# Kernel optimization log

Hardware: AMD Instinct MI355X
Metric: run time of the kernel (lower is better)

## Reference

```python
import jax, jax.numpy as jnp
import numpy as np

GCN_DIM = 512
POS_EMB_DIM = 64
K = 8
L = 128  # uttr_len
B = 16
PAIR_FEAT = 2 * GCN_DIM + POS_EMB_DIM


def _pair_indices(L, K):
    # Static (trace-time) construction of the windowed pair list, matching the
    # torch masked_select over the full L*L pair grid: row p = i*L + j keeps
    # pairs with |j - i| <= K, in the same row-major order.
    i = np.repeat(np.arange(L), L)
    j = np.tile(np.arange(L), L)
    rel = j - i
    mask = np.abs(rel) <= K
    return i[mask], j[mask], rel[mask]


def setup_inputs() -> dict:
    key = jax.random.key(0)
    k1, k2, k3, k4, k5, k6, k7 = jax.random.split(key, 7)
    h_emo = jax.random.normal(k1, (B, L, GCN_DIM), dtype=jnp.float32)
    h_cause = jax.random.normal(k2, (B, L, GCN_DIM), dtype=jnp.float32)
    # xavier_uniform for embedding table
    lim_e = np.sqrt(6.0 / (2 * K + 1 + POS_EMB_DIM))
    pos_emb = jax.random.uniform(k3, (2 * K + 1, POS_EMB_DIM), minval=-lim_e, maxval=lim_e, dtype=jnp.float32)
    lim1 = np.sqrt(1.0 / PAIR_FEAT)
    W1 = jax.random.uniform(k4, (PAIR_FEAT, PAIR_FEAT), minval=-lim1, maxval=lim1, dtype=jnp.float32)
    b1 = jax.random.uniform(k5, (PAIR_FEAT,), minval=-lim1, maxval=lim1, dtype=jnp.float32)
    W2 = jax.random.uniform(k6, (1, PAIR_FEAT), minval=-lim1, maxval=lim1, dtype=jnp.float32)
    b2 = jax.random.uniform(k7, (1,), minval=-lim1, maxval=lim1, dtype=jnp.float32)
    return {
        "uttr_output_h_emotion": h_emo,
        "uttr_output_h_cause": h_cause,
        "pos_emb": pos_emb,
        "W1": W1,
        "b1": b1,
        "W2": W2,
        "b2": b2,
    }


def reference(uttr_output_h_emotion, uttr_output_h_cause, pos_emb, W1, b1, W2, b2):
    emo_idx, cau_idx, rel_np = _pair_indices(L, K)  # static numpy, length n
    emo_idx_j = jnp.asarray(emo_idx)
    cau_idx_j = jnp.asarray(cau_idx)
    rel = jnp.asarray(rel_np)  # [n], values in [-K, K]

    # windowed pair gather: couples_h = [H_emo[i] ; H_cause[j]]  -> [B, n, 2*g]
    P = jnp.concatenate(
        [uttr_output_h_emotion[:, emo_idx_j, :], uttr_output_h_cause[:, cau_idx_j, :]],
        axis=2,
    )

    # relative-position embedding + Gaussian kernel smoothing (batch-invariant)
    rel_emb = pos_emb[rel + K]  # [n, pos_emb_dim]
    rel_f = rel.astype(jnp.float32)
    kernel = jnp.exp(-jnp.square(rel_f[:, None] - rel_f[None, :]))  # [n, n]
    smoothed = kernel @ rel_emb  # [n, pos_emb_dim]

    couples = jnp.concatenate(
        [P, jnp.broadcast_to(smoothed[None], (P.shape[0],) + smoothed.shape)], axis=2
    )  # [B, n, PAIR_FEAT]

    h = jax.nn.relu(jnp.einsum("bnf,gf->bng", couples, W1) + b1)
    pred = (jnp.einsum("bnf,of->bno", h, W2) + b2).squeeze(-1)  # [B, n]

    emo_cau_pos = jnp.stack([emo_idx_j + 1, cau_idx_j + 1], axis=1)  # [n, 2], int
    return pred, emo_cau_pos
```

## Files before the change

kernel.cpp:

```cpp
#include <hip/hip_runtime.h>

typedef unsigned short u16;
typedef unsigned int u32;
typedef __attribute__((ext_vector_type(4))) float f32x4;
typedef __attribute__((ext_vector_type(8))) __bf16 bf16x8;
typedef __attribute__((ext_vector_type(4))) u16 u16x4;
typedef __attribute__((ext_vector_type(4))) float f32x4v;

#define LSEQ 128
#define KW 8
#define NP 2104
#define BATCH 16
#define MTOT 33664
#define FDIM 1088
#define GPAD 1152

#define WS_W1P  0ul
#define WS_EMOB 2506752ul
#define WS_CAUB 4603904ul
#define WS_SB   6701056ul
#define WS_TABI 6775040ul
#define WS_TABJ 6783456ul
#define WS_TABR 6791872ul
#define WS_EC   6800288ul

__device__ __forceinline__ u16 f2bf(float x) {
  union { float f; u32 u; } v; v.f = x;
  u32 r = v.u + 0x7fffu + ((v.u >> 16) & 1u);
  return (u16)(r >> 16);
}

__device__ __forceinline__ void load_lds16(const void* g, void* l) {
  __builtin_amdgcn_global_load_lds(
      (const __attribute__((address_space(1))) void*)g,
      (__attribute__((address_space(3))) void*)l, 16, 0, 0);
}

__global__ __launch_bounds__(256)
void setup_all(const float* __restrict__ emo, const float* __restrict__ cau,
               const float* __restrict__ pos_emb, const float* __restrict__ W1,
               const float* __restrict__ b1,
               u16* __restrict__ W1p, u16* __restrict__ emoB,
               u16* __restrict__ cauB, float* __restrict__ Sb,
               int* __restrict__ tab_i, int* __restrict__ tab_j,
               int* __restrict__ tab_r, float* __restrict__ out_pos) {
  __shared__ float smL[17 * 64];
  const int bx = blockIdx.x;
  const int t = threadIdx.x;
  if (bx < 1224) {
    int idx = bx * 256 + t;
    if (idx >= 313344) return;
    int g = idx / 272;
    int f = (idx - g * 272) * 4;
    u16x4 o;
    if (g < 1088) {
      f32x4v v = *(const f32x4v*)&W1[g * 1088 + f];
      o.x = f2bf(v.x); o.y = f2bf(v.y); o.z = f2bf(v.z); o.w = f2bf(v.w);
    } else {
      o.x = 0; o.y = 0; o.z = 0; o.w = 0;
    }
    *(u16x4*)&W1p[(size_t)g * 1088 + f] = o;
  } else if (bx < 3272) {
    int idx = (bx - 1224) * 256 + t;
    if (idx < 262144) {
      f32x4v v = *(const f32x4v*)&emo[idx * 4];
      u16x4 o; o.x = f2bf(v.x); o.y = f2bf(v.y); o.z = f2bf(v.z); o.w = f2bf(v.w);
      *(u16x4*)&emoB[idx * 4] = o;
    } else {
      int k = idx - 262144;
      f32x4v v = *(const f32x4v*)&cau[k * 4];
      u16x4 o; o.x = f2bf(v.x); o.y = f2bf(v.y); o.z = f2bf(v.z); o.w = f2bf(v.w);
      *(u16x4*)&cauB[k * 4] = o;
    }
  } else if (bx == 3272) {
    if (t < LSEQ) {
      int i = t;
      int off = 0;
      for (int tt = 0; tt < i; ++tt) {
        int lo = tt - KW; if (lo < 0) lo = 0;
        int hi = tt + KW; if (hi > LSEQ - 1) hi = LSEQ - 1;
        off += hi - lo + 1;
      }
      int jlo = i - KW; if (jlo < 0) jlo = 0;
      int jhi = i + KW; if (jhi > LSEQ - 1) jhi = LSEQ - 1;
      for (int j = jlo; j <= jhi; ++j) {
        int p = off + (j - jlo);
        tab_i[p] = i; tab_j[p] = j; tab_r[p] = j - i;
        out_pos[2 * p]     = (float)(i + 1);
        out_pos[2 * p + 1] = (float)(j + 1);
      }
    }
  } else {
    for (int idx = t; idx < 17 * 64; idx += 256) {
      int r = idx >> 6, d = idx & 63;
      float acc = 0.f;
      for (int s = 0; s < 17; ++s) {
        float diff = (float)(r - s);
        int a = s - 8; if (a < 0) a = -a;
        float cnt = (float)(128 - a);
        acc += cnt * expf(-diff * diff) * pos_emb[s * 64 + d];
      }
      smL[idx] = acc;
    }
    __syncthreads();
    int idx2 = (bx - 3273) * 256 + t;
    if (idx2 < 17 * 1088) {
      int r = idx2 / 1088;
      int g = idx2 - r * 1088;
      float a = b1[g];
      const float* wr = &W1[(size_t)g * 1088 + 1024];
      const float* sr = &smL[r * 64];
#pragma unroll 8
      for (int d = 0; d < 64; ++d) a = fmaf(sr[d], wr[d], a);
      Sb[r * 1088 + g] = a;
    }
  }
}

__global__ __launch_bounds__(256, 2)
void feat_gemm(const u16* __restrict__ emoB, const u16* __restrict__ cauB,
               const u16* __restrict__ W1p, float* __restrict__ EC) {
  __shared__ __align__(16) u16 As[128 * 32];
  __shared__ __align__(16) u16 Bs[128 * 32];

  const int tid = threadIdx.x;
  const int mblk = blockIdx.x;
  const int gbase = blockIdx.y * 128;

  const int lane = tid & 63;
  const int w = tid >> 6;
  const int lrow = lane & 15;
  const int lk = (lane >> 4) * 8;
  const int wm = (w >> 1) * 64;
  const int wn = (w & 1) * 64;

  const int row0 = tid >> 2;
  const int sub = (tid & 3) * 8;

  const u16* Asrc = (mblk < 16) ? emoB : cauB;
  const int arow = (mblk & 15) * 128;
  const int fsel = (mblk < 16) ? 0 : 512;

  const u32 a0 = (u32)(arow + row0) * 512 + sub;
  const u32 a1 = a0 + 64 * 512;
  const u32 b0 = (u32)(gbase + row0) * 1088 + fsel + sub;
  const u32 b1o = b0 + 64 * 1088;

  char* AsB = (char*)&As[0] + w * 1024;
  char* BsB = (char*)&Bs[0] + w * 1024;

  f32x4 acc[4][4];
#pragma unroll
  for (int mi = 0; mi < 4; ++mi)
#pragma unroll
    for (int ni = 0; ni < 4; ++ni) acc[mi][ni] = (f32x4){0.f, 0.f, 0.f, 0.f};

  for (int ks = 0; ks < 16; ++ks) {
    const int f0 = ks * 32;
    load_lds16(Asrc + a0 + f0, AsB);
    load_lds16(Asrc + a1 + f0, AsB + 4096);
    load_lds16(W1p + b0 + f0, BsB);
    load_lds16(W1p + b1o + f0, BsB + 4096);
    __syncthreads();

    bf16x8 av[4], bv[4];
#pragma unroll
    for (int mi = 0; mi < 4; ++mi)
      av[mi] = *(const bf16x8*)&As[(wm + mi * 16 + lrow) * 32 + lk];
#pragma unroll
    for (int ni = 0; ni < 4; ++ni)
      bv[ni] = *(const bf16x8*)&Bs[(wn + ni * 16 + lrow) * 32 + lk];
#pragma unroll
    for (int mi = 0; mi < 4; ++mi)
#pragma unroll
      for (int ni = 0; ni < 4; ++ni)
        acc[mi][ni] = __builtin_amdgcn_mfma_f32_16x16x32_bf16(av[mi], bv[ni], acc[mi][ni], 0, 0, 0);
    __syncthreads();
  }

  const int rbase = mblk * 128 + wm + ((lane >> 4) << 2);
#pragma unroll
  for (int mi = 0; mi < 4; ++mi) {
#pragma unroll
    for (int ni = 0; ni < 4; ++ni) {
      const int ocol = gbase + wn + ni * 16 + lrow;
      float* dst = EC + (size_t)(rbase + mi * 16) * GPAD + ocol;
#pragma unroll
      for (int r2 = 0; r2 < 4; ++r2) dst[(size_t)r2 * GPAD] = acc[mi][ni][r2];
    }
  }
}

__global__ __launch_bounds__(256)
void combine(const float* __restrict__ EC, const float* __restrict__ Sb,
             const float* __restrict__ W2, const float* __restrict__ b2,
             const int* __restrict__ tab_i, const int* __restrict__ tab_j,
             const int* __restrict__ tab_r, float* __restrict__ pred) {
  const int bid = blockIdx.x;
  const int sb = (bid & 7) * 1052 + (bid >> 3);
  const int w = threadIdx.x >> 6;
  const int lane = threadIdx.x & 63;
  const int q = sb * 4 + w;
  const int b = q / NP;
  const int p = q - b * NP;
  const int i = tab_i[p];
  const int j = tab_j[p];
  const int r = tab_r[p];

  const float* e = EC + (size_t)(b * LSEQ + i) * GPAD;
  const float* c = EC + (size_t)(2048 + b * LSEQ + j) * GPAD;
  const float* s = Sb + (r + KW) * FDIM;

  f32x4v acc = {0.f, 0.f, 0.f, 0.f};
#pragma unroll
  for (int it = 0; it < 4; ++it) {
    const int g = it * 256 + (lane << 2);
    f32x4v ev = *(const f32x4v*)(e + g);
    f32x4v cv = *(const f32x4v*)(c + g);
    f32x4v sv = *(const f32x4v*)(s + g);
    f32x4v wv = *(const f32x4v*)(W2 + g);
    float v0 = fmaxf(ev.x + cv.x + sv.x, 0.f);
    float v1 = fmaxf(ev.y + cv.y + sv.y, 0.f);
    float v2 = fmaxf(ev.z + cv.z + sv.z, 0.f);
    float v3 = fmaxf(ev.w + cv.w + sv.w, 0.f);
    acc.x = fmaf(v0, wv.x, acc.x);
    acc.y = fmaf(v1, wv.y, acc.y);
    acc.z = fmaf(v2, wv.z, acc.z);
    acc.w = fmaf(v3, wv.w, acc.w);
  }
  float a = acc.x + acc.y + acc.z + acc.w;
  {
    const int g = 1024 + lane;
    float v = fmaxf(e[g] + c[g] + s[g], 0.f);
    a = fmaf(v, W2[g], a);
  }
  a += __shfl_xor(a, 1);
  a += __shfl_xor(a, 2);
  a += __shfl_xor(a, 4);
  a += __shfl_xor(a, 8);
  a += __shfl_xor(a, 16);
  a += __shfl_xor(a, 32);
  if (lane == 0) pred[q] = a + b2[0];
}

extern "C" void kernel_launch(void* const* d_in, const int* in_sizes, int n_in,
                              void* d_out, int out_size, void* d_ws, size_t ws_size,
                              hipStream_t stream) {
  const float* h_emo = (const float*)d_in[0];
  const float* h_cau = (const float*)d_in[1];
  const float* pos_emb = (const float*)d_in[2];
  const float* W1 = (const float*)d_in[3];
  const float* b1 = (const float*)d_in[4];
  const float* W2 = (const float*)d_in[5];
  const float* b2 = (const float*)d_in[6];

  char* ws = (char*)d_ws;
  u16* W1p = (u16*)(ws + WS_W1P);
  u16* emoB = (u16*)(ws + WS_EMOB);
  u16* cauB = (u16*)(ws + WS_CAUB);
  float* Sb = (float*)(ws + WS_SB);
  int* tab_i = (int*)(ws + WS_TABI);
  int* tab_j = (int*)(ws + WS_TABJ);
  int* tab_r = (int*)(ws + WS_TABR);
  float* EC = (float*)(ws + WS_EC);

  float* pred = (float*)d_out;
  float* out_pos = (float*)d_out + MTOT;

  setup_all<<<3346, 256, 0, stream>>>(h_emo, h_cau, pos_emb, W1, b1,
                                      W1p, emoB, cauB, Sb,
                                      tab_i, tab_j, tab_r, out_pos);
  feat_gemm<<<dim3(32, 9), 256, 0, stream>>>(emoB, cauB, W1p, EC);
  combine<<<8416, 256, 0, stream>>>(EC, Sb, W2, b2, tab_i, tab_j, tab_r, pred);
}
```

Baseline: 120.3 us.

## Restructure combine per query row with LDS-staged bf16 bias table and smaller GEMM tiles

The combine kernel now assigns one emotion row i per pair of waves. Each wave keeps its E row and W2 slice in registers and iterates over the window of cause rows j with a software-prefetched next row. The 17x1088 smoothed-bias table is stored as bf16 and staged into LDS per block, replacing per-pair index tables with a single row-offset table. The feature GEMM M tile is halved to 64 rows to double the block count and raise occupancy. This cuts redundant E and W2 global reads and raises GEMM parallelism, at the cost of bf16 rounding on the bias term, a large LDS allocation per combine block, and serial loops inside each block.

```diff
diff --git a/kernel.cpp b/kernel.cpp
--- a/kernel.cpp
+++ b/kernel.cpp
@@ -19,15 +19,17 @@
 #define WS_EMOB 2506752ul
 #define WS_CAUB 4603904ul
 #define WS_SB   6701056ul
-#define WS_TABI 6775040ul
-#define WS_TABJ 6783456ul
-#define WS_TABR 6791872ul
-#define WS_EC   6800288ul
+#define WS_TOFF 6738048ul
+#define WS_EC   6738560ul
 
 __device__ __forceinline__ u16 f2bf(float x) {
   union { float f; u32 u; } v; v.f = x;
   u32 r = v.u + 0x7fffu + ((v.u >> 16) & 1u);
   return (u16)(r >> 16);
+}
+
+__device__ __forceinline__ float bf2f(u16 x) {
+  union { u32 u; float f; } v; v.u = ((u32)x) << 16; return v.f;
 }
 
 __device__ __forceinline__ void load_lds16(const void* g, void* l) {
@@ -41,9 +43,8 @@
                const float* __restrict__ pos_emb, const float* __restrict__ W1,
                const float* __restrict__ b1,
                u16* __restrict__ W1p, u16* __restrict__ emoB,
-               u16* __restrict__ cauB, float* __restrict__ Sb,
-               int* __restrict__ tab_i, int* __restrict__ tab_j,
-               int* __restrict__ tab_r, float* __restrict__ out_pos) {
+               u16* __restrict__ cauB, u16* __restrict__ Sb,
+               int* __restrict__ tab_off, float* __restrict__ out_pos) {
   __shared__ float smL[17 * 64];
   const int bx = blockIdx.x;
   const int t = threadIdx.x;
@@ -81,11 +82,11 @@
         int hi = tt + KW; if (hi > LSEQ - 1) hi = LSEQ - 1;
         off += hi - lo + 1;
       }
+      tab_off[i] = off;
       int jlo = i - KW; if (jlo < 0) jlo = 0;
       int jhi = i + KW; if (jhi > LSEQ - 1) jhi = LSEQ - 1;
       for (int j = jlo; j <= jhi; ++j) {
         int p = off + (j - jlo);
-        tab_i[p] = i; tab_j[p] = j; tab_r[p] = j - i;
         out_pos[2 * p]     = (float)(i + 1);
         out_pos[2 * p + 1] = (float)(j + 1);
       }
@@ -112,15 +113,15 @@
       const float* sr = &smL[r * 64];
 #pragma unroll 8
       for (int d = 0; d < 64; ++d) a = fmaf(sr[d], wr[d], a);
-      Sb[r * 1088 + g] = a;
-    }
-  }
-}
-
-__global__ __launch_bounds__(256, 2)
+      Sb[r * 1088 + g] = f2bf(a);
+    }
+  }
+}
+
+__global__ __launch_bounds__(256, 4)
 void feat_gemm(const u16* __restrict__ emoB, const u16* __restrict__ cauB,
                const u16* __restrict__ W1p, float* __restrict__ EC) {
-  __shared__ __align__(16) u16 As[128 * 32];
+  __shared__ __align__(16) u16 As[64 * 32];
   __shared__ __align__(16) u16 Bs[128 * 32];
 
   const int tid = threadIdx.x;
@@ -131,56 +132,54 @@
   const int w = tid >> 6;
   const int lrow = lane & 15;
   const int lk = (lane >> 4) * 8;
-  const int wm = (w >> 1) * 64;
+  const int wm = (w >> 1) * 32;
   const int wn = (w & 1) * 64;
 
   const int row0 = tid >> 2;
   const int sub = (tid & 3) * 8;
 
-  const u16* Asrc = (mblk < 16) ? emoB : cauB;
-  const int arow = (mblk & 15) * 128;
-  const int fsel = (mblk < 16) ? 0 : 512;
+  const u16* Asrc = (mblk < 32) ? emoB : cauB;
+  const int arow = (mblk & 31) * 64;
+  const int fsel = (mblk < 32) ? 0 : 512;
 
   const u32 a0 = (u32)(arow + row0) * 512 + sub;
-  const u32 a1 = a0 + 64 * 512;
   const u32 b0 = (u32)(gbase + row0) * 1088 + fsel + sub;
-  const u32 b1o = b0 + 64 * 1088;
-
-  char* AsB = (char*)&As[0] + w * 1024;
-  char* BsB = (char*)&Bs[0] + w * 1024;
-
-  f32x4 acc[4][4];
-#pragma unroll
-  for (int mi = 0; mi < 4; ++mi)
+  const u32 b1o = b0 + 64u * 1088;
+
+  char* AsD = (char*)&As[0] + tid * 16;
+  char* BsD = (char*)&Bs[0] + tid * 16;
+
+  f32x4 acc[2][4];
+#pragma unroll
+  for (int mi = 0; mi < 2; ++mi)
 #pragma unroll
     for (int ni = 0; ni < 4; ++ni) acc[mi][ni] = (f32x4){0.f, 0.f, 0.f, 0.f};
 
   for (int ks = 0; ks < 16; ++ks) {
     const int f0 = ks * 32;
-    load_lds16(Asrc + a0 + f0, AsB);
-    load_lds16(Asrc + a1 + f0, AsB + 4096);
-    load_lds16(W1p + b0 + f0, BsB);
-    load_lds16(W1p + b1o + f0, BsB + 4096);
+    load_lds16(Asrc + a0 + f0, AsD);
+    load_lds16(W1p + b0 + f0, BsD);
+    load_lds16(W1p + b1o + f0, BsD + 4096);
     __syncthreads();
 
-    bf16x8 av[4], bv[4];
-#pragma unroll
-    for (int mi = 0; mi < 4; ++mi)
+    bf16x8 av[2], bv[4];
+#pragma unroll
+    for (int mi = 0; mi < 2; ++mi)
       av[mi] = *(const bf16x8*)&As[(wm + mi * 16 + lrow) * 32 + lk];
 #pragma unroll
     for (int ni = 0; ni < 4; ++ni)
       bv[ni] = *(const bf16x8*)&Bs[(wn + ni * 16 + lrow) * 32 + lk];
 #pragma unroll
-    for (int mi = 0; mi < 4; ++mi)
+    for (int mi = 0; mi < 2; ++mi)
 #pragma unroll
       for (int ni = 0; ni < 4; ++ni)
         acc[mi][ni] = __builtin_amdgcn_mfma_f32_16x16x32_bf16(av[mi], bv[ni], acc[mi][ni], 0, 0, 0);
     __syncthreads();
   }
 
-  const int rbase = mblk * 128 + wm + ((lane >> 4) << 2);
-#pragma unroll
-  for (int mi = 0; mi < 4; ++mi) {
+  const int rbase = mblk * 64 + wm + ((lane >> 4) << 2);
+#pragma unroll
+  for (int mi = 0; mi < 2; ++mi) {
 #pragma unroll
     for (int ni = 0; ni < 4; ++ni) {
       const int ocol = gbase + wn + ni * 16 + lrow;
@@ -191,56 +190,110 @@
   }
 }
 
-__global__ __launch_bounds__(256)
-void combine(const float* __restrict__ EC, const float* __restrict__ Sb,
+__global__ __launch_bounds__(256, 4)
+void combine(const float* __restrict__ EC, const u16* __restrict__ Sb,
              const float* __restrict__ W2, const float* __restrict__ b2,
-             const int* __restrict__ tab_i, const int* __restrict__ tab_j,
-             const int* __restrict__ tab_r, float* __restrict__ pred) {
+             const int* __restrict__ tab_off, float* __restrict__ pred) {
+  __shared__ __align__(16) u16 Sl[17 * 1088];
+  __shared__ float partA[2][17], partB[2][17];
+
+  const int tid = threadIdx.x;
   const int bid = blockIdx.x;
-  const int sb = (bid & 7) * 1052 + (bid >> 3);
-  const int w = threadIdx.x >> 6;
-  const int lane = threadIdx.x & 63;
-  const int q = sb * 4 + w;
-  const int b = q / NP;
-  const int p = q - b * NP;
-  const int i = tab_i[p];
-  const int j = tab_j[p];
-  const int r = tab_r[p];
-
-  const float* e = EC + (size_t)(b * LSEQ + i) * GPAD;
-  const float* c = EC + (size_t)(2048 + b * LSEQ + j) * GPAD;
-  const float* s = Sb + (r + KW) * FDIM;
-
-  f32x4v acc = {0.f, 0.f, 0.f, 0.f};
-#pragma unroll
-  for (int it = 0; it < 4; ++it) {
-    const int g = it * 256 + (lane << 2);
-    f32x4v ev = *(const f32x4v*)(e + g);
-    f32x4v cv = *(const f32x4v*)(c + g);
-    f32x4v sv = *(const f32x4v*)(s + g);
-    f32x4v wv = *(const f32x4v*)(W2 + g);
-    float v0 = fmaxf(ev.x + cv.x + sv.x, 0.f);
-    float v1 = fmaxf(ev.y + cv.y + sv.y, 0.f);
-    float v2 = fmaxf(ev.z + cv.z + sv.z, 0.f);
-    float v3 = fmaxf(ev.w + cv.w + sv.w, 0.f);
-    acc.x = fmaf(v0, wv.x, acc.x);
-    acc.y = fmaf(v1, wv.y, acc.y);
-    acc.z = fmaf(v2, wv.z, acc.z);
-    acc.w = fmaf(v3, wv.w, acc.w);
-  }
-  float a = acc.x + acc.y + acc.z + acc.w;
+  const int sb = (bid & 7) * 128 + (bid >> 3);
+
   {
-    const int g = 1024 + lane;
-    float v = fmaxf(e[g] + c[g] + s[g], 0.f);
-    a = fmaf(v, W2[g], a);
-  }
-  a += __shfl_xor(a, 1);
-  a += __shfl_xor(a, 2);
-  a += __shfl_xor(a, 4);
-  a += __shfl_xor(a, 8);
-  a += __shfl_xor(a, 16);
-  a += __shfl_xor(a, 32);
-  if (lane == 0) pred[q] = a + b2[0];
+    char* dst = (char*)&Sl[0];
+    const char* src = (const char*)Sb;
+#pragma unroll
+    for (int it = 0; it < 9; ++it)
+      load_lds16(src + it * 4096 + tid * 16, dst + it * 4096 + tid * 16);
+    if (tid < 8)
+      load_lds16(src + 36864 + tid * 16, dst + 36864 + tid * 16);
+  }
+
+  const int w = tid >> 6;
+  const int lane = tid & 63;
+  const int h = w >> 1;
+  const int gh = w & 1;
+  const int u = sb * 2 + h;
+  const int b = u >> 7;
+  const int i = u & 127;
+  int jlo = i - KW; if (jlo < 0) jlo = 0;
+  int jhi = i + KW; if (jhi > 127) jhi = 127;
+
+  const float bias2 = b2[0];
+  const float* Erow = EC + (size_t)(b * 128 + i) * GPAD;
+  const float* Cbase = EC + (size_t)(2048 + b * 128) * GPAD;
+
+  const int g0 = gh * 512 + lane * 4;
+  const int g1 = g0 + 256;
+  const f32x4v e0 = *(const f32x4v*)(Erow + g0);
+  const f32x4v e1 = *(const f32x4v*)(Erow + g1);
+  const f32x4v w20 = *(const f32x4v*)(W2 + g0);
+  const f32x4v w21 = *(const f32x4v*)(W2 + g1);
+  float eT = 0.f, w2T = 0.f;
+  if (gh) { eT = Erow[1024 + lane]; w2T = W2[1024 + lane]; }
+
+  __syncthreads();
+
+  const float* Crow = Cbase + (size_t)jlo * GPAD;
+  f32x4v c0 = *(const f32x4v*)(Crow + g0);
+  f32x4v c1 = *(const f32x4v*)(Crow + g1);
+  float cT = gh ? Crow[1024 + lane] : 0.f;
+
+  for (int j = jlo; j <= jhi; ++j) {
+    f32x4v n0 = c0, n1 = c1; float nT = cT;
+    if (j < jhi) {
+      const float* Nrow = Cbase + (size_t)(j + 1) * GPAD;
+      n0 = *(const f32x4v*)(Nrow + g0);
+      n1 = *(const f32x4v*)(Nrow + g1);
+      if (gh) nT = Nrow[1024 + lane];
+    }
+    const int r = j - i + KW;
+    const u16* srow = &Sl[r * 1088];
+    u16x4 sa = *(const u16x4*)(srow + g0);
+    u16x4 sc = *(const u16x4*)(srow + g1);
+
+    float a = 0.f;
+    a = fmaf(fmaxf(e0.x + c0.x + bf2f(sa.x), 0.f), w20.x, a);
+    a = fmaf(fmaxf(e0.y + c0.y + bf2f(sa.y), 0.f), w20.y, a);
+    a = fmaf(fmaxf(e0.z + c0.z + bf2f(sa.z), 0.f), w20.z, a);
+    a = fmaf(fmaxf(e0.w + c0.w + bf2f(sa.w), 0.f), w20.w, a);
+    a = fmaf(fmaxf(e1.x + c1.x + bf2f(sc.x), 0.f), w21.x, a);
+    a = fmaf(fmaxf(e1.y + c1.y + bf2f(sc.y), 0.f), w21.y, a);
+    a = fmaf(fmaxf(e1.z + c1.z + bf2f(sc.z), 0.f), w21.z, a);
+    a = fmaf(fmaxf(e1.w + c1.w + bf2f(sc.w), 0.f), w21.w, a);
+    if (gh) {
+      float sT = bf2f(srow[1024 + lane]);
+      a = fmaf(fmaxf(eT + cT + sT, 0.f), w2T, a);
+    }
+
+    a += __shfl_xor(a, 1);
+    a += __shfl_xor(a, 2);
+    a += __shfl_xor(a, 4);
+    a += __shfl_xor(a, 8);
+    a += __shfl_xor(a, 16);
+    a += __shfl_xor(a, 32);
+    if (lane == 0) {
+      if (gh) partB[h][j - jlo] = a;
+      else    partA[h][j - jlo] = a;
+    }
+    c0 = n0; c1 = n1; cT = nT;
+  }
+  __syncthreads();
+
+  if (w < 2) {
+    const int u2 = sb * 2 + w;
+    const int bb = u2 >> 7;
+    const int i2 = u2 & 127;
+    int jl2 = i2 - KW; if (jl2 < 0) jl2 = 0;
+    int jh2 = i2 + KW; if (jh2 > 127) jh2 = 127;
+    const int cnt2 = jh2 - jl2 + 1;
+    if (lane < cnt2) {
+      const int q = bb * NP + tab_off[i2] + lane;
+      pred[q] = partA[w][lane] + partB[w][lane] + bias2;
+    }
+  }
 }
 
 extern "C" void kernel_launch(void* const* d_in, const int* in_sizes, int n_in,
@@ -258,18 +311,15 @@
   u16* W1p = (u16*)(ws + WS_W1P);
   u16* emoB = (u16*)(ws + WS_EMOB);
   u16* cauB = (u16*)(ws + WS_CAUB);
-  float* Sb = (float*)(ws + WS_SB);
-  int* tab_i = (int*)(ws + WS_TABI);
-  int* tab_j = (int*)(ws + WS_TABJ);
-  int* tab_r = (int*)(ws + WS_TABR);
+  u16* Sb = (u16*)(ws + WS_SB);
+  int* tab_off = (int*)(ws + WS_TOFF);
   float* EC = (float*)(ws + WS_EC);
 
   float* pred = (float*)d_out;
   float* out_pos = (float*)d_out + MTOT;
 
   setup_all<<<3346, 256, 0, stream>>>(h_emo, h_cau, pos_emb, W1, b1,
-                                      W1p, emoB, cauB, Sb,
-                                      tab_i, tab_j, tab_r, out_pos);
-  feat_gemm<<<dim3(32, 9), 256, 0, stream>>>(emoB, cauB, W1p, EC);
-  combine<<<8416, 256, 0, stream>>>(EC, Sb, W2, b2, tab_i, tab_j, tab_r, pred);
-}
+                                      W1p, emoB, cauB, Sb, tab_off, out_pos);
+  feat_gemm<<<dim3(64, 9), 256, 0, stream>>>(emoB, cauB, W1p, EC);
+  combine<<<1024, 256, 0, stream>>>(EC, Sb, W2, b2, tab_off, pred);
+}
```

New measurement: 109.9 us. -8.6%, faster.

## Fuse feature GEMM with pairwise combine using LDS tiles and atomic output accumulation

Applied to the files above, without the earlier changes.

Replaces the separate feature GEMM and combine kernels with one kernel. Each block computes a 32-row emotion tile and a 48-row halo cause tile for one 128-column slice of W1, keeps them in LDS, and reduces the windowed pairs in place. Partial dot products go to pred through atomicAdd, with pred pre-initialised to b2 in setup. The smoothed bias table is stored as bf16. This removes the large fp32 EC intermediate round trip through global memory and one kernel launch. In exchange it recomputes the halo cause rows, adds atomics and float-order nondeterminism, and runs at lower MFMA utilisation per block.

```diff
diff --git a/kernel.cpp b/kernel.cpp
--- a/kernel.cpp
+++ b/kernel.cpp
@@ -10,7 +10,6 @@
 #define LSEQ 128
 #define KW 8
 #define NP 2104
-#define BATCH 16
 #define MTOT 33664
 #define FDIM 1088
 #define GPAD 1152
@@ -19,10 +18,8 @@
 #define WS_EMOB 2506752ul
 #define WS_CAUB 4603904ul
 #define WS_SB   6701056ul
-#define WS_TABI 6775040ul
-#define WS_TABJ 6783456ul
-#define WS_TABR 6791872ul
-#define WS_EC   6800288ul
+#define WS_W2P  6740224ul
+#define WS_TOFF 6744832ul
 
 __device__ __forceinline__ u16 f2bf(float x) {
   union { float f; u32 u; } v; v.f = x;
@@ -30,6 +27,10 @@
   return (u16)(r >> 16);
 }
 
+__device__ __forceinline__ float bf2f(u16 x) {
+  union { u32 u; float f; } v; v.u = ((u32)x) << 16; return v.f;
+}
+
 __device__ __forceinline__ void load_lds16(const void* g, void* l) {
   __builtin_amdgcn_global_load_lds(
       (const __attribute__((address_space(1))) void*)g,
@@ -39,11 +40,12 @@
 __global__ __launch_bounds__(256)
 void setup_all(const float* __restrict__ emo, const float* __restrict__ cau,
                const float* __restrict__ pos_emb, const float* __restrict__ W1,
-               const float* __restrict__ b1,
+               const float* __restrict__ b1, const float* __restrict__ W2,
+               const float* __restrict__ b2,
                u16* __restrict__ W1p, u16* __restrict__ emoB,
-               u16* __restrict__ cauB, float* __restrict__ Sb,
-               int* __restrict__ tab_i, int* __restrict__ tab_j,
-               int* __restrict__ tab_r, float* __restrict__ out_pos) {
+               u16* __restrict__ cauB, u16* __restrict__ Sb,
+               float* __restrict__ W2p, int* __restrict__ tab_off,
+               float* __restrict__ pred, float* __restrict__ out_pos) {
   __shared__ float smL[17 * 64];
   const int bx = blockIdx.x;
   const int t = threadIdx.x;
@@ -81,16 +83,18 @@
         int hi = tt + KW; if (hi > LSEQ - 1) hi = LSEQ - 1;
         off += hi - lo + 1;
       }
+      tab_off[i] = off;
       int jlo = i - KW; if (jlo < 0) jlo = 0;
       int jhi = i + KW; if (jhi > LSEQ - 1) jhi = LSEQ - 1;
       for (int j = jlo; j <= jhi; ++j) {
         int p = off + (j - jlo);
-        tab_i[p] = i; tab_j[p] = j; tab_r[p] = j - i;
         out_pos[2 * p]     = (float)(i + 1);
         out_pos[2 * p + 1] = (float)(j + 1);
       }
     }
-  } else {
+    for (int g = t; g < GPAD; g += 256)
+      W2p[g] = (g < FDIM) ? W2[g] : 0.f;
+  } else if (bx < 3350) {
     for (int idx = t; idx < 17 * 64; idx += 256) {
       int r = idx >> 6, d = idx & 63;
       float acc = 0.f;
@@ -104,143 +108,180 @@
     }
     __syncthreads();
     int idx2 = (bx - 3273) * 256 + t;
-    if (idx2 < 17 * 1088) {
-      int r = idx2 / 1088;
-      int g = idx2 - r * 1088;
-      float a = b1[g];
-      const float* wr = &W1[(size_t)g * 1088 + 1024];
-      const float* sr = &smL[r * 64];
+    if (idx2 < 17 * GPAD) {
+      int r = idx2 / GPAD;
+      int g = idx2 - r * GPAD;
+      u16 ov = 0;
+      if (g < FDIM) {
+        float a = b1[g];
+        const float* wr = &W1[(size_t)g * 1088 + 1024];
+        const float* sr = &smL[r * 64];
 #pragma unroll 8
-      for (int d = 0; d < 64; ++d) a = fmaf(sr[d], wr[d], a);
-      Sb[r * 1088 + g] = a;
+        for (int d = 0; d < 64; ++d) a = fmaf(sr[d], wr[d], a);
+        ov = f2bf(a);
+      }
+      Sb[idx2] = ov;
+    }
+  } else {
+    int k = (bx - 3350) * 256 + t;
+    if (k < 8416) {
+      float bv = b2[0];
+      f32x4v o = {bv, bv, bv, bv};
+      *(f32x4v*)&pred[k * 4] = o;
     }
   }
 }
 
 __global__ __launch_bounds__(256, 2)
-void feat_gemm(const u16* __restrict__ emoB, const u16* __restrict__ cauB,
-               const u16* __restrict__ W1p, float* __restrict__ EC) {
-  __shared__ __align__(16) u16 As[128 * 32];
+void fused_pair(const u16* __restrict__ emoB, const u16* __restrict__ cauB,
+                const u16* __restrict__ W1p, const u16* __restrict__ Sb,
+                const float* __restrict__ W2p, const int* __restrict__ tab_off,
+                float* __restrict__ pred) {
+  __shared__ __align__(16) u16 As[48 * 32];
   __shared__ __align__(16) u16 Bs[128 * 32];
+  __shared__ __align__(16) float Et[32 * 132];
+  __shared__ __align__(16) float Ct[48 * 132];
+  __shared__ u16 Sl[17 * 136];
+  __shared__ int toff[32];
 
   const int tid = threadIdx.x;
-  const int mblk = blockIdx.x;
-  const int gbase = blockIdx.y * 128;
+  const int id = blockIdx.x;
+  const int sid = (id & 7) * 72 + (id >> 3);
+  const int mblk = sid / 9;
+  const int gt = sid - mblk * 9;
+  const int b = mblk >> 2;
+  const int lo = (mblk & 3) * 32;
+  const int cb = lo - 8;
+  const int gbase = gt * 128;
 
   const int lane = tid & 63;
   const int w = tid >> 6;
   const int lrow = lane & 15;
   const int lk = (lane >> 4) * 8;
-  const int wm = (w >> 1) * 64;
-  const int wn = (w & 1) * 64;
-
-  const int row0 = tid >> 2;
-  const int sub = (tid & 3) * 8;
-
-  const u16* Asrc = (mblk < 16) ? emoB : cauB;
-  const int arow = (mblk & 15) * 128;
-  const int fsel = (mblk < 16) ? 0 : 512;
-
-  const u32 a0 = (u32)(arow + row0) * 512 + sub;
-  const u32 a1 = a0 + 64 * 512;
-  const u32 b0 = (u32)(gbase + row0) * 1088 + fsel + sub;
-  const u32 b1o = b0 + 64 * 1088;
-
-  char* AsB = (char*)&As[0] + w * 1024;
-  char* BsB = (char*)&Bs[0] + w * 1024;
-
-  f32x4 acc[4][4];
-#pragma unroll
-  for (int mi = 0; mi < 4; ++mi)
-#pragma unroll
-    for (int ni = 0; ni < 4; ++ni) acc[mi][ni] = (f32x4){0.f, 0.f, 0.f, 0.f};
-
+  const int wmE = (w >> 1) * 16;
+  const int wnE = (w & 1) * 64;
+
+  for (int u = tid; u < 272; u += 256) {
+    const int r = u >> 4, cu = u & 15;
+    const u16* src = &Sb[r * GPAD + gbase + cu * 8];
+    u16x4 v0 = *(const u16x4*)src;
+    u16x4 v1 = *(const u16x4*)(src + 4);
+    *(u16x4*)&Sl[r * 136 + cu * 8] = v0;
+    *(u16x4*)&Sl[r * 136 + cu * 8 + 4] = v1;
+  }
+  if (tid < 32) toff[tid] = tab_off[lo + tid];
+
+  const int srow = tid >> 2;
+  const int ssub = (tid & 3) * 8;
+  const u16* aE = emoB + ((size_t)(b * LSEQ + lo) << 9);
+  const u16* bW = W1p + (size_t)gbase * FDIM;
+
+  f32x4 accE[4];
+#pragma unroll
+  for (int x = 0; x < 4; ++x) accE[x] = (f32x4){0.f, 0.f, 0.f, 0.f};
   for (int ks = 0; ks < 16; ++ks) {
-    const int f0 = ks * 32;
-    load_lds16(Asrc + a0 + f0, AsB);
-    load_lds16(Asrc + a1 + f0, AsB + 4096);
-    load_lds16(W1p + b0 + f0, BsB);
-    load_lds16(W1p + b1o + f0, BsB + 4096);
-    __syncthreads();
-
-    bf16x8 av[4], bv[4];
-#pragma unroll
-    for (int mi = 0; mi < 4; ++mi)
-      av[mi] = *(const bf16x8*)&As[(wm + mi * 16 + lrow) * 32 + lk];
-#pragma unroll
-    for (int ni = 0; ni < 4; ++ni)
-      bv[ni] = *(const bf16x8*)&Bs[(wn + ni * 16 + lrow) * 32 + lk];
-#pragma unroll
-    for (int mi = 0; mi < 4; ++mi)
-#pragma unroll
-      for (int ni = 0; ni < 4; ++ni)
-        acc[mi][ni] = __builtin_amdgcn_mfma_f32_16x16x32_bf16(av[mi], bv[ni], acc[mi][ni], 0, 0, 0);
-    __syncthreads();
-  }
-
-  const int rbase = mblk * 128 + wm + ((lane >> 4) << 2);
-#pragma unroll
-  for (int mi = 0; mi < 4; ++mi) {
+    const int kofs = ks * 32;
+    if (tid < 128) load_lds16(aE + srow * 512 + kofs + ssub, (char*)&As[0] + tid * 16);
+    load_lds16(bW + srow * FDIM + kofs + ssub, (char*)&Bs[0] + tid * 16);
+    load_lds16(bW + (srow + 64) * FDIM + kofs + ssub, (char*)&Bs[0] + tid * 16 + 4096);
+    __syncthreads();
+    bf16x8 av = *(const bf16x8*)&As[(wmE + lrow) * 32 + lk];
 #pragma unroll
     for (int ni = 0; ni < 4; ++ni) {
-      const int ocol = gbase + wn + ni * 16 + lrow;
-      float* dst = EC + (size_t)(rbase + mi * 16) * GPAD + ocol;
-#pragma unroll
-      for (int r2 = 0; r2 < 4; ++r2) dst[(size_t)r2 * GPAD] = acc[mi][ni][r2];
-    }
-  }
-}
-
-__global__ __launch_bounds__(256)
-void combine(const float* __restrict__ EC, const float* __restrict__ Sb,
-             const float* __restrict__ W2, const float* __restrict__ b2,
-             const int* __restrict__ tab_i, const int* __restrict__ tab_j,
-             const int* __restrict__ tab_r, float* __restrict__ pred) {
-  const int bid = blockIdx.x;
-  const int sb = (bid & 7) * 1052 + (bid >> 3);
-  const int w = threadIdx.x >> 6;
-  const int lane = threadIdx.x & 63;
-  const int q = sb * 4 + w;
-  const int b = q / NP;
-  const int p = q - b * NP;
-  const int i = tab_i[p];
-  const int j = tab_j[p];
-  const int r = tab_r[p];
-
-  const float* e = EC + (size_t)(b * LSEQ + i) * GPAD;
-  const float* c = EC + (size_t)(2048 + b * LSEQ + j) * GPAD;
-  const float* s = Sb + (r + KW) * FDIM;
-
-  f32x4v acc = {0.f, 0.f, 0.f, 0.f};
-#pragma unroll
-  for (int it = 0; it < 4; ++it) {
-    const int g = it * 256 + (lane << 2);
-    f32x4v ev = *(const f32x4v*)(e + g);
-    f32x4v cv = *(const f32x4v*)(c + g);
-    f32x4v sv = *(const f32x4v*)(s + g);
-    f32x4v wv = *(const f32x4v*)(W2 + g);
-    float v0 = fmaxf(ev.x + cv.x + sv.x, 0.f);
-    float v1 = fmaxf(ev.y + cv.y + sv.y, 0.f);
-    float v2 = fmaxf(ev.z + cv.z + sv.z, 0.f);
-    float v3 = fmaxf(ev.w + cv.w + sv.w, 0.f);
-    acc.x = fmaf(v0, wv.x, acc.x);
-    acc.y = fmaf(v1, wv.y, acc.y);
-    acc.z = fmaf(v2, wv.z, acc.z);
-    acc.w = fmaf(v3, wv.w, acc.w);
-  }
-  float a = acc.x + acc.y + acc.z + acc.w;
+      bf16x8 bvv = *(const bf16x8*)&Bs[(wnE + ni * 16 + lrow) * 32 + lk];
+      accE[ni] = __builtin_amdgcn_mfma_f32_16x16x32_bf16(av, bvv, accE[ni], 0, 0, 0);
+    }
+    __syncthreads();
+  }
   {
-    const int g = 1024 + lane;
-    float v = fmaxf(e[g] + c[g] + s[g], 0.f);
-    a = fmaf(v, W2[g], a);
-  }
-  a += __shfl_xor(a, 1);
-  a += __shfl_xor(a, 2);
-  a += __shfl_xor(a, 4);
-  a += __shfl_xor(a, 8);
-  a += __shfl_xor(a, 16);
-  a += __shfl_xor(a, 32);
-  if (lane == 0) pred[q] = a + b2[0];
+    const int mr = wmE + (lane >> 4) * 4;
+#pragma unroll
+    for (int ni = 0; ni < 4; ++ni) {
+      const int n = wnE + ni * 16 + lrow;
+#pragma unroll
+      for (int r2 = 0; r2 < 4; ++r2)
+        Et[(mr + r2) * 132 + n] = accE[ni][r2];
+    }
+  }
+
+  f32x4 accC[6];
+#pragma unroll
+  for (int x = 0; x < 6; ++x) accC[x] = (f32x4){0.f, 0.f, 0.f, 0.f};
+  const int f0 = w * 6;
+  const int rfL = f0 >> 3;
+  const int rfH = (f0 + 5) >> 3;
+  int csr = cb + srow;
+  csr = (csr < 0) ? 0 : (csr > 127 ? 127 : csr);
+  const u16* aC = cauB + ((size_t)(b * LSEQ) << 9);
+  for (int ks = 0; ks < 16; ++ks) {
+    const int kofs = ks * 32;
+    if (tid < 192) load_lds16(aC + csr * 512 + kofs + ssub, (char*)&As[0] + tid * 16);
+    load_lds16(bW + srow * FDIM + 512 + kofs + ssub, (char*)&Bs[0] + tid * 16);
+    load_lds16(bW + (srow + 64) * FDIM + 512 + kofs + ssub, (char*)&Bs[0] + tid * 16 + 4096);
+    __syncthreads();
+    bf16x8 avL = *(const bf16x8*)&As[(rfL * 16 + lrow) * 32 + lk];
+    bf16x8 avH = *(const bf16x8*)&As[(rfH * 16 + lrow) * 32 + lk];
+#pragma unroll
+    for (int t = 0; t < 6; ++t) {
+      const int f = f0 + t;
+      bf16x8 av = ((f >> 3) == rfL) ? avL : avH;
+      bf16x8 bvv = *(const bf16x8*)&Bs[((f & 7) * 16 + lrow) * 32 + lk];
+      accC[t] = __builtin_amdgcn_mfma_f32_16x16x32_bf16(av, bvv, accC[t], 0, 0, 0);
+    }
+    __syncthreads();
+  }
+  {
+#pragma unroll
+    for (int t = 0; t < 6; ++t) {
+      const int f = f0 + t;
+      const int m = (f >> 3) * 16 + (lane >> 4) * 4;
+      const int n = (f & 7) * 16 + lrow;
+#pragma unroll
+      for (int r2 = 0; r2 < 4; ++r2)
+        Ct[(m + r2) * 132 + n] = accC[t][r2];
+    }
+  }
+  __syncthreads();
+
+  const int lg = lane >> 4;
+  const int li = lane & 15;
+  const float* w2g = W2p + gbase + li * 8;
+  const f32x4v w2a = *(const f32x4v*)w2g;
+  const f32x4v w2b = *(const f32x4v*)(w2g + 4);
+  const int ib0 = w * 8;
+  for (int ii = 0; ii < 8; ++ii) {
+    const int il = ib0 + ii;
+    const int i = lo + il;
+    const f32x4v e0 = *(const f32x4v*)&Et[il * 132 + li * 8];
+    const f32x4v e1 = *(const f32x4v*)&Et[il * 132 + li * 8 + 4];
+    const int jlo_i = (i >= KW) ? (i - KW) : 0;
+    const int qb = b * NP + toff[il] - jlo_i;
+#pragma unroll
+    for (int jt = 0; jt < 5; ++jt) {
+      const int j = (jt < 4) ? (i - KW + jt * 4 + lg) : (i + KW);
+      const int crow = (j - cb) * 132;
+      const f32x4v c0 = *(const f32x4v*)&Ct[crow + li * 8];
+      const f32x4v c1 = *(const f32x4v*)&Ct[crow + li * 8 + 4];
+      const int r = j - i + KW;
+      const u16* sp = &Sl[r * 136 + li * 8];
+      const u16x4 s0 = *(const u16x4*)sp;
+      const u16x4 s1 = *(const u16x4*)(sp + 4);
+      float a = fmaxf(e0.x + c0.x + bf2f(s0.x), 0.f) * w2a.x;
+      a = fmaf(fmaxf(e0.y + c0.y + bf2f(s0.y), 0.f), w2a.y, a);
+      a = fmaf(fmaxf(e0.z + c0.z + bf2f(s0.z), 0.f), w2a.z, a);
+      a = fmaf(fmaxf(e0.w + c0.w + bf2f(s0.w), 0.f), w2a.w, a);
+      a = fmaf(fmaxf(e1.x + c1.x + bf2f(s1.x), 0.f), w2b.x, a);
+      a = fmaf(fmaxf(e1.y + c1.y + bf2f(s1.y), 0.f), w2b.y, a);
+      a = fmaf(fmaxf(e1.z + c1.z + bf2f(s1.z), 0.f), w2b.z, a);
+      a = fmaf(fmaxf(e1.w + c1.w + bf2f(s1.w), 0.f), w2b.w, a);
+      a += __shfl_xor(a, 1, 16);
+      a += __shfl_xor(a, 2, 16);
+      a += __shfl_xor(a, 4, 16);
+      a += __shfl_xor(a, 8, 16);
+      const bool valid = (j >= 0) && (j <= 127) && (jt < 4 || lg == 0);
+      if (li == 0 && valid) atomicAdd(&pred[qb + j], a);
+    }
+  }
 }
 
 extern "C" void kernel_launch(void* const* d_in, const int* in_sizes, int n_in,
@@ -258,18 +299,15 @@
   u16* W1p = (u16*)(ws + WS_W1P);
   u16* emoB = (u16*)(ws + WS_EMOB);
   u16* cauB = (u16*)(ws + WS_CAUB);
-  float* Sb = (float*)(ws + WS_SB);
-  int* tab_i = (int*)(ws + WS_TABI);
-  int* tab_j = (int*)(ws + WS_TABJ);
-  int* tab_r = (int*)(ws + WS_TABR);
-  float* EC = (float*)(ws + WS_EC);
+  u16* Sb = (u16*)(ws + WS_SB);
+  float* W2p = (float*)(ws + WS_W2P);
+  int* tab_off = (int*)(ws + WS_TOFF);
 
   float* pred = (float*)d_out;
   float* out_pos = (float*)d_out + MTOT;
 
-  setup_all<<<3346, 256, 0, stream>>>(h_emo, h_cau, pos_emb, W1, b1,
-                                      W1p, emoB, cauB, Sb,
-                                      tab_i, tab_j, tab_r, out_pos);
-  feat_gemm<<<dim3(32, 9), 256, 0, stream>>>(emoB, cauB, W1p, EC);
-  combine<<<8416, 256, 0, stream>>>(EC, Sb, W2, b2, tab_i, tab_j, tab_r, pred);
-}
+  setup_all<<<3383, 256, 0, stream>>>(h_emo, h_cau, pos_emb, W1, b1, W2, b2,
+                                      W1p, emoB, cauB, Sb, W2p, tab_off,
+                                      pred, out_pos);
+  fused_pair<<<576, 256, 0, stream>>>(emoB, cauB, W1p, Sb, W2p, tab_off, pred);
+}
```

Result: slower. 127.3 us (+5.8%).
